# Optimization experiments

Measured on AMD Instinct MI355X. Metric: run time of the kernel, lower is better.

## Reference

```python
import jax, jax.numpy as jnp
import numpy as np

B, S, E = 2, 2048, 1024
H, NQ = 16, 8          # n_heads, n_qubits
D = E // H             # head_dim


def setup_inputs() -> dict:
    key = jax.random.key(0)
    ks = jax.random.split(key, 11)
    sc = 0.02
    return {
        "query": jax.random.normal(ks[0], (B, S, E), jnp.float32),
        "key":   jax.random.normal(ks[1], (B, S, E), jnp.float32),
        "value": jax.random.normal(ks[2], (B, S, E), jnp.float32),
        "Wq": jax.random.normal(ks[3], (E, NQ), jnp.float32) * sc,
        "bq": jnp.zeros((NQ,), jnp.float32),
        "Wk": jax.random.normal(ks[4], (E, NQ), jnp.float32) * sc,
        "bk": jnp.zeros((NQ,), jnp.float32),
        "Wv": jax.random.normal(ks[5], (E, E), jnp.float32) * sc,
        "bv": jnp.zeros((E,), jnp.float32),
        "Wo": jax.random.normal(ks[6], (E, E), jnp.float32) * sc,
        "bo": jnp.zeros((E,), jnp.float32),
    }


def reference(query, key, value, Wq, bq, Wk, bk, Wv, bv, Wo, bo):
    # Linear encoders (q/k are computed in the original but, because
    # _apply_rotation is the identity, they never influence the scores).
    q = query @ Wq + bq            # [B,S,NQ] (dead math, kept for fidelity)
    k = key @ Wk + bk              # [B,S,NQ]
    v = value @ Wv + bv            # [B,S,E]
    v = v.reshape(B, S, H, D).transpose(0, 2, 1, 3)  # [B,H,S,D]

    # Quantum overlap: both encoded states are always |0>, so
    # |<q_state|k_state>|^2 == 1 for every (b,i,j) pair.
    scores = jnp.full((B, H, S, S), 1.0 / np.sqrt(NQ), dtype=query.dtype)
    attn = jax.nn.softmax(scores, axis=-1)           # uniform 1/S weights

    out = jnp.einsum('bhij,bhjd->bhid', attn, v)     # [B,H,S,D]
    out = out.transpose(0, 2, 1, 3).reshape(B, S, E)
    out = out @ Wo + bo
    return out, attn
```

## Files before the change

kernel.cpp:

```cpp
#include <hip/hip_runtime.h>


typedef float floatx4 __attribute__((ext_vector_type(4)));
typedef float floatx2 __attribute__((ext_vector_type(2)));

#define ATTN_BASE4 1048576LL
#define O1 0
#define F1 7168
#define O2 7168
#define F2 8800
#define O3 15968
#define F3 9380
#define O4 25348
#define F4 7420

__device__ __forceinline__ void fill_chunks(float* __restrict__ out,
                                            int fb, int nf, int O, int F) {
    floatx4* o4 = (floatx4*)out;
    const floatx4 av = (floatx4)(1.0f / 2048.0f);
    for (int c = fb; c < F; c += nf) {
        long long base = ATTN_BASE4 + ((long long)(O + c) << 10) + threadIdx.x;
        #pragma unroll
        for (int it = 0; it < 4; ++it)
            __builtin_nontemporal_store(av, &o4[base + it * 256]);
    }
}

__global__ void __launch_bounds__(256)
k1_colsum_fill(const float* __restrict__ value,
               float* __restrict__ part1, float* __restrict__ out) {
    int blk = blockIdx.x, t = threadIdx.x;
    if (blk < 256) {
        int b = blk >> 7, sp = blk & 127;
        const floatx4* v4 = (const floatx4*)value;
        floatx4 acc = (floatx4)0.0f;
        int rowbase = b * 2048 + sp * 16;
        #pragma unroll
        for (int r = 0; r < 16; ++r)
            acc += v4[(size_t)(rowbase + r) * 256 + t];
        ((floatx4*)part1)[(size_t)(b * 128 + sp) * 256 + t] = acc;
    } else {
        fill_chunks(out, blk - 256, 1792, O1, F1);
    }
}

__global__ void __launch_bounds__(256)
k2_zpart_fill(const float* __restrict__ part1, const float* __restrict__ Wv,
              float* __restrict__ zpart, float* __restrict__ out) {
    int blk = blockIdx.x, t = threadIdx.x;
    if (blk < 128) {
        __shared__ float red[256];
        __shared__ float vsl[32];
        int b = blk >> 6, r = blk & 63, ks = r >> 1, eh = r & 1;
        int k0 = ks * 32;
        int kl = t & 31, sg = t >> 5;
        float s = 0.f;
        #pragma unroll
        for (int i = 0; i < 16; ++i) {
            int sp = sg * 16 + i;
            s += part1[(size_t)(b * 128 + sp) * 1024 + k0 + kl];
        }
        red[t] = s;
        __syncthreads();
        if (t < 32) {
            float v = 0.f;
            #pragma unroll
            for (int g = 0; g < 8; ++g) v += red[g * 32 + t];
            vsl[t] = v * (1.0f / 2048.0f);
        }
        __syncthreads();
        int e2 = eh * 512 + 2 * t;
        floatx2 acc = (floatx2)0.0f;
        #pragma unroll 8
        for (int kk = 0; kk < 32; ++kk) {
            floatx2 w = *(const floatx2*)&Wv[(size_t)(k0 + kk) * 1024 + e2];
            acc += vsl[kk] * w;
        }
        *(floatx2*)&zpart[(size_t)(b * 32 + ks) * 1024 + e2] = acc;
    } else {
        fill_chunks(out, blk - 128, 1920, O2, F2);
    }
}

__global__ void __launch_bounds__(256)
k3_zfin_fill(const float* __restrict__ zpart, const float* __restrict__ bv,
             float* __restrict__ z, float* __restrict__ out) {
    int blk = blockIdx.x, t = threadIdx.x;
    if (blk < 64) {
        int b = blk >> 5, es = blk & 31, e0 = es * 32;
        if (t < 32) {
            float s = bv[e0 + t];
            #pragma unroll 8
            for (int seg = 0; seg < 32; ++seg)
                s += zpart[(size_t)(b * 32 + seg) * 1024 + e0 + t];
            z[b * 1024 + e0 + t] = s;
        }
    } else {
        fill_chunks(out, blk - 64, 1984, O3, F3);
    }
}

__global__ void __launch_bounds__(256)
k4_orow_bcast_fill(const float* __restrict__ z, const float* __restrict__ Wo,
                   const float* __restrict__ bo, float* __restrict__ out) {
    int blk = blockIdx.x, t = threadIdx.x;
    if (blk < 1024) {
        __shared__ __align__(16) float zsh[1024];
        __shared__ float red[256];
        __shared__ __align__(16) float orow[16];
        int b = blk >> 9, r = blk & 511, cg = r >> 3, rr = r & 7;
        int e0 = cg * 16;
        ((floatx4*)zsh)[t] = ((const floatx4*)z)[b * 256 + t];
        __syncthreads();
        int eo = e0 + (t & 15), sg = t >> 4;
        float part = 0.f;
        int eb = sg * 64;
        #pragma unroll 8
        for (int ee = 0; ee < 64; ++ee) {
            int e = eb + ee;
            part += zsh[e] * Wo[(size_t)e * 1024 + eo];
        }
        red[t] = part;
        __syncthreads();
        if (t < 16) {
            float o = bo[e0 + t];
            #pragma unroll
            for (int g = 0; g < 16; ++g) o += red[g * 16 + t];
            orow[t] = o;
        }
        __syncthreads();
        int q = t & 3, rl = t >> 2;
        floatx4 w = ((const floatx4*)orow)[q];
        floatx4* o4 = (floatx4*)out;
        size_t cb = (size_t)(e0 >> 2) + q;
        int rbase = rr * 256;
        #pragma unroll
        for (int i = 0; i < 4; ++i) {
            int row = rbase + i * 64 + rl;
            __builtin_nontemporal_store(w, &o4[((size_t)b * 2048 + row) * 256 + cb]);
        }
    } else {
        fill_chunks(out, blk - 1024, 1024, O4, F4);
    }
}

extern "C" void kernel_launch(void* const* d_in, const int* in_sizes, int n_in,
                              void* d_out, int out_size, void* d_ws, size_t ws_size,
                              hipStream_t stream) {
    const float* value = (const float*)d_in[2];
    const float* Wv    = (const float*)d_in[7];
    const float* bv    = (const float*)d_in[8];
    const float* Wo    = (const float*)d_in[9];
    const float* bo    = (const float*)d_in[10];
    float* out = (float*)d_out;

    float* part1 = (float*)d_ws;
    float* zpart = part1 + 262144;
    float* zbuf  = zpart + 65536;

    k1_colsum_fill    <<<2048, 256, 0, stream>>>(value, part1, out);
    k2_zpart_fill     <<<2048, 256, 0, stream>>>(part1, Wv, zpart, out);
    k3_zfin_fill      <<<2048, 256, 0, stream>>>(zpart, bv, zbuf, out);
    k4_orow_bcast_fill<<<2048, 256, 0, stream>>>(zbuf, Wo, bo, out);
}
```

Before: 109.2 us.

## Fuse four kernels into one persistent kernel with global atomic barriers

```diff
diff --git a/kernel.cpp b/kernel.cpp
--- a/kernel.cpp
+++ b/kernel.cpp
@@ -4,32 +4,49 @@
 typedef float floatx4 __attribute__((ext_vector_type(4)));
 typedef float floatx2 __attribute__((ext_vector_type(2)));
 
-#define ATTN_BASE4 1048576LL
-#define O1 0
-#define F1 7168
-#define O2 7168
-#define F2 8800
-#define O3 15968
-#define F3 9380
-#define O4 25348
-#define F4 7420
+#define NBLK 512u
 
-__device__ __forceinline__ void fill_chunks(float* __restrict__ out,
-                                            int fb, int nf, int O, int F) {
+__device__ __forceinline__ void fill_run(float* __restrict__ out, int c0, int n) {
     floatx4* o4 = (floatx4*)out;
     const floatx4 av = (floatx4)(1.0f / 2048.0f);
-    for (int c = fb; c < F; c += nf) {
-        long long base = ATTN_BASE4 + ((long long)(O + c) << 10) + threadIdx.x;
+    for (int j = 0; j < n; ++j) {
+        long long base = 1048576LL + ((long long)(c0 + j) << 10) + threadIdx.x;
         #pragma unroll
         for (int it = 0; it < 4; ++it)
             __builtin_nontemporal_store(av, &o4[base + it * 256]);
     }
 }
 
-__global__ void __launch_bounds__(256)
-k1_colsum_fill(const float* __restrict__ value,
-               float* __restrict__ part1, float* __restrict__ out) {
+__device__ __forceinline__ void gbar(unsigned int* ctr, unsigned int target) {
+    __syncthreads();
+    if (threadIdx.x == 0) {
+        __threadfence();
+        __hip_atomic_fetch_add(ctr, 1u, __ATOMIC_RELEASE, __HIP_MEMORY_SCOPE_AGENT);
+        long long guard = 0;
+        while (__hip_atomic_load(ctr, __ATOMIC_ACQUIRE, __HIP_MEMORY_SCOPE_AGENT)
+               < target) {
+            __builtin_amdgcn_s_sleep(2);
+            if (++guard > (1LL << 26)) break;
+        }
+        __threadfence();
+    }
+    __syncthreads();
+}
+
+__global__ void __launch_bounds__(256, 2)
+fused_all(const float* __restrict__ value,
+          const float* __restrict__ Wv, const float* __restrict__ bv,
+          const float* __restrict__ Wo, const float* __restrict__ bo,
+          float* __restrict__ part1, float* __restrict__ zpart,
+          float* __restrict__ z, unsigned int* __restrict__ ctr,
+          float* __restrict__ out)
+{
     int blk = blockIdx.x, t = threadIdx.x;
+    __shared__ float red[256];
+    __shared__ float vsl[32];
+    __shared__ __align__(16) float zsh[1024];
+    __shared__ __align__(16) float orow[16];
+
     if (blk < 256) {
         int b = blk >> 7, sp = blk & 127;
         const floatx4* v4 = (const floatx4*)value;
@@ -40,26 +57,18 @@
             acc += v4[(size_t)(rowbase + r) * 256 + t];
         ((floatx4*)part1)[(size_t)(b * 128 + sp) * 256 + t] = acc;
     } else {
-        fill_chunks(out, blk - 256, 1792, O1, F1);
+        fill_run(out, (blk - 256) * 4, 4);
     }
-}
+    gbar(ctr, NBLK);
 
-__global__ void __launch_bounds__(256)
-k2_zpart_fill(const float* __restrict__ part1, const float* __restrict__ Wv,
-              float* __restrict__ zpart, float* __restrict__ out) {
-    int blk = blockIdx.x, t = threadIdx.x;
     if (blk < 128) {
-        __shared__ float red[256];
-        __shared__ float vsl[32];
         int b = blk >> 6, r = blk & 63, ks = r >> 1, eh = r & 1;
         int k0 = ks * 32;
         int kl = t & 31, sg = t >> 5;
         float s = 0.f;
         #pragma unroll
-        for (int i = 0; i < 16; ++i) {
-            int sp = sg * 16 + i;
-            s += part1[(size_t)(b * 128 + sp) * 1024 + k0 + kl];
-        }
+        for (int i = 0; i < 16; ++i)
+            s += part1[(size_t)(b * 128 + sg * 16 + i) * 1024 + k0 + kl];
         red[t] = s;
         __syncthreads();
         if (t < 32) {
@@ -72,20 +81,14 @@
         int e2 = eh * 512 + 2 * t;
         floatx2 acc = (floatx2)0.0f;
         #pragma unroll 8
-        for (int kk = 0; kk < 32; ++kk) {
-            floatx2 w = *(const floatx2*)&Wv[(size_t)(k0 + kk) * 1024 + e2];
-            acc += vsl[kk] * w;
-        }
+        for (int kk = 0; kk < 32; ++kk)
+            acc += vsl[kk] * *(const floatx2*)&Wv[(size_t)(k0 + kk) * 1024 + e2];
         *(floatx2*)&zpart[(size_t)(b * 32 + ks) * 1024 + e2] = acc;
     } else {
-        fill_chunks(out, blk - 128, 1920, O2, F2);
+        fill_run(out, 1024 + (blk - 128) * 5, 5);
     }
-}
+    gbar(ctr, 2 * NBLK);
 
-__global__ void __launch_bounds__(256)
-k3_zfin_fill(const float* __restrict__ zpart, const float* __restrict__ bv,
-             float* __restrict__ z, float* __restrict__ out) {
-    int blk = blockIdx.x, t = threadIdx.x;
     if (blk < 64) {
         int b = blk >> 5, es = blk & 31, e0 = es * 32;
         if (t < 32) {
@@ -95,31 +98,21 @@
                 s += zpart[(size_t)(b * 32 + seg) * 1024 + e0 + t];
             z[b * 1024 + e0 + t] = s;
         }
-    } else {
-        fill_chunks(out, blk - 64, 1984, O3, F3);
     }
-}
+    fill_run(out, 2944 + blk * 40, 40);
+    gbar(ctr, 3 * NBLK);
 
-__global__ void __launch_bounds__(256)
-k4_orow_bcast_fill(const float* __restrict__ z, const float* __restrict__ Wo,
-                   const float* __restrict__ bo, float* __restrict__ out) {
-    int blk = blockIdx.x, t = threadIdx.x;
-    if (blk < 1024) {
-        __shared__ __align__(16) float zsh[1024];
-        __shared__ float red[256];
-        __shared__ __align__(16) float orow[16];
-        int b = blk >> 9, r = blk & 511, cg = r >> 3, rr = r & 7;
-        int e0 = cg * 16;
+    {
+        int b = blk >> 8, r = blk & 255, cgp = r >> 2, rr = r & 3;
+        int e0 = cgp * 16;
         ((floatx4*)zsh)[t] = ((const floatx4*)z)[b * 256 + t];
         __syncthreads();
         int eo = e0 + (t & 15), sg = t >> 4;
         float part = 0.f;
         int eb = sg * 64;
         #pragma unroll 8
-        for (int ee = 0; ee < 64; ++ee) {
-            int e = eb + ee;
-            part += zsh[e] * Wo[(size_t)e * 1024 + eo];
-        }
+        for (int ee = 0; ee < 64; ++ee)
+            part += zsh[eb + ee] * Wo[(size_t)(eb + ee) * 1024 + eo];
         red[t] = part;
         __syncthreads();
         if (t < 16) {
@@ -133,15 +126,15 @@
         floatx4 w = ((const floatx4*)orow)[q];
         floatx4* o4 = (floatx4*)out;
         size_t cb = (size_t)(e0 >> 2) + q;
-        int rbase = rr * 256;
+        int rbase = rr * 512;
         #pragma unroll
-        for (int i = 0; i < 4; ++i) {
+        for (int i = 0; i < 8; ++i) {
             int row = rbase + i * 64 + rl;
             __builtin_nontemporal_store(w, &o4[((size_t)b * 2048 + row) * 256 + cb]);
         }
-    } else {
-        fill_chunks(out, blk - 1024, 1024, O4, F4);
     }
+    if (blk < 128) fill_run(out, 23424 + blk * 19, 19);
+    else           fill_run(out, 25856 + (blk - 128) * 18, 18);
 }
 
 extern "C" void kernel_launch(void* const* d_in, const int* in_sizes, int n_in,
@@ -157,9 +150,9 @@
     float* part1 = (float*)d_ws;
     float* zpart = part1 + 262144;
     float* zbuf  = zpart + 65536;
+    unsigned int* ctr = (unsigned int*)(zbuf + 2048 + 64);
 
-    k1_colsum_fill    <<<2048, 256, 0, stream>>>(value, part1, out);
-    k2_zpart_fill     <<<2048, 256, 0, stream>>>(part1, Wv, zpart, out);
-    k3_zfin_fill      <<<2048, 256, 0, stream>>>(zpart, bv, zbuf, out);
-    k4_orow_bcast_fill<<<2048, 256, 0, stream>>>(zbuf, Wo, bo, out);
+    hipMemsetAsync(ctr, 0, 16, stream);
+    fused_all<<<NBLK, 256, 0, stream>>>(value, Wv, bv, Wo, bo,
+                                        part1, zpart, zbuf, ctr, out);
 }
```

After: 399.7 us. +266.0%, slower.
